# Optimization experiments

Measured on AMD Instinct MI355X. Metric: run time of the kernel, lower is better.

Reference implementation:

```python
import jax, jax.numpy as jnp
import numpy as np

N_NODES = 50000
N_EDGES = 1_250_000
D_FEAT = 64


def setup_inputs() -> dict:
    key = jax.random.key(0)
    k_seq, k_rows, k_cols, k_vals = jax.random.split(key, 4)
    seq = jax.random.normal(k_seq, (1, N_NODES, D_FEAT), dtype=jnp.float32)
    rows = jnp.sort(jax.random.randint(k_rows, (N_EDGES,), 0, N_NODES, dtype=jnp.int32))
    cols = jax.random.randint(k_cols, (N_EDGES,), 0, N_NODES, dtype=jnp.int32)
    vals = jax.random.uniform(k_vals, (N_EDGES,), dtype=jnp.float32)
    return {"seq": seq, "vals": vals, "rows": rows, "cols": cols}


def reference(seq, vals, rows, cols):
    # torch.spmm(adj, seq.squeeze(0)) with adj in COO form (rows, cols, vals):
    # out[r] = sum_{e: rows[e]==r} vals[e] * seq[0, cols[e], :]
    x = jnp.squeeze(seq, 0)                      # [N, D]
    gathered = x[cols] * vals[:, None]           # [E, D] gather + scale
    out = jax.ops.segment_sum(gathered, rows, num_segments=N_NODES)  # [N, D]
    return out[None]                             # unsqueeze(0) -> [1, N, D]
```

## Files before the change

kernel.cpp:

```cpp
#include <hip/hip_runtime.h>


#define WPB 4
#define RPW 8

typedef float  f32x4 __attribute__((ext_vector_type(4)));

__global__ __launch_bounds__(256) void prep_kernel(
    const float4* __restrict__ seq,
    uint2*        __restrict__ seqt,
    const int*    __restrict__ rows,
    int*          __restrict__ row_start,
    int n_nodes, int n_edges, int cvt_blocks)
{
    if ((int)blockIdx.x < cvt_blocks) {
        const int t = blockIdx.x * 256 + threadIdx.x;
        if (t >= n_nodes * 16) return;
        const float4 f = seq[t];
        const unsigned ux = __float_as_uint(f.x), uy = __float_as_uint(f.y);
        const unsigned uz = __float_as_uint(f.z), uw = __float_as_uint(f.w);
        const unsigned bx = (ux + 0x7FFFu + ((ux >> 16) & 1u)) >> 16;
        const unsigned by = (uy + 0x7FFFu + ((uy >> 16) & 1u)) >> 16;
        const unsigned bz = (uz + 0x7FFFu + ((uz >> 16) & 1u)) >> 16;
        const unsigned bw = (uw + 0x7FFFu + ((uw >> 16) & 1u)) >> 16;
        uint2 o;
        o.x = bx | (by << 16);
        o.y = bz | (bw << 16);
        const int n = t >> 4;
        const int h = (t >> 3) & 1;
        const int q = t & 7;
        seqt[(size_t)h * (size_t)n_nodes * 8 + n * 8 + q] = o;
    } else {
        const int e = (blockIdx.x - cvt_blocks) * 256 + threadIdx.x;
        if (e >= n_edges) return;
        const int r    = rows[e];
        const int prev = (e == 0) ? -1 : rows[e - 1];
        for (int t = prev + 1; t <= r; ++t) row_start[t] = e;
        if (e == n_edges - 1)
            for (int t = r + 1; t <= n_nodes; ++t) row_start[t] = n_edges;
    }
}

__global__ __launch_bounds__(256) void spmm_kernel(
    const uint2* __restrict__ seqt,
    const float* __restrict__ vals,
    const int*   __restrict__ cols,
    const int*   __restrict__ row_start,
    float*       __restrict__ out,
    int n_nodes, int n_edges)
{
    const int lane = threadIdx.x & 63;
    const int sub  = lane >> 3;
    const int fl   = lane & 7;

    const int h      = blockIdx.x & 1;
    const int rowblk = blockIdx.x >> 1;
    const int wave   = rowblk * WPB + (threadIdx.x >> 6);

    const int r = wave * RPW + sub;
    if (wave * RPW >= n_nodes) return;
    const bool valid = (r < n_nodes);

    int e = 0, e_end = 0;
    if (valid) {
        e     = row_start[r];
        e_end = row_start[r + 1];
    }

    const uint2* __restrict__ base = seqt + (size_t)h * (size_t)n_nodes * 8;

    float4 acc = make_float4(0.f, 0.f, 0.f, 0.f);

    while (__any(e < e_end)) {
        int cidx = e + fl;
        cidx = (cidx < 0) ? 0 : (cidx >= n_edges ? n_edges - 1 : cidx);
        const int   c = __builtin_nontemporal_load(cols + cidx);
        const float v = __builtin_nontemporal_load(vals + cidx);

        uint2 x[8];
#pragma unroll
        for (int u = 0; u < 8; ++u) {
            const int cu = __shfl(c, (sub << 3) | u);
            if (e + u < e_end)
                x[u] = base[(cu << 3) + fl];
        }
#pragma unroll
        for (int u = 0; u < 8; ++u) {
            const float vu = __shfl(v, (sub << 3) | u);
            if (e + u < e_end) {
                const float f0 = __uint_as_float(x[u].x << 16);
                const float f1 = __uint_as_float(x[u].x & 0xFFFF0000u);
                const float f2 = __uint_as_float(x[u].y << 16);
                const float f3 = __uint_as_float(x[u].y & 0xFFFF0000u);
                acc.x = fmaf(vu, f0, acc.x);
                acc.y = fmaf(vu, f1, acc.y);
                acc.z = fmaf(vu, f2, acc.z);
                acc.w = fmaf(vu, f3, acc.w);
            }
        }
        e += 8;
    }

    if (valid) {
        f32x4 o;
        o.x = acc.x; o.y = acc.y; o.z = acc.z; o.w = acc.w;
        __builtin_nontemporal_store(
            o, (f32x4*)out + ((r << 4) + (h << 3) + fl));
    }
}

extern "C" void kernel_launch(void* const* d_in, const int* in_sizes, int n_in,
                              void* d_out, int out_size, void* d_ws, size_t ws_size,
                              hipStream_t stream) {
    const float* seq  = (const float*)d_in[0];
    const float* vals = (const float*)d_in[1];
    const int*   rows = (const int*)d_in[2];
    const int*   cols = (const int*)d_in[3];
    float*       out  = (float*)d_out;

    const int n_edges = in_sizes[1];
    const int n_nodes = out_size / 64;

    int*   row_start = (int*)d_ws;
    size_t off       = (((size_t)(n_nodes + 1) * 4 + 255) / 256) * 256;
    uint2* seqt      = (uint2*)((char*)d_ws + off);

    {
        const int cvt_blocks = (n_nodes * 16 + 255) / 256;
        const int rp_blocks  = (n_edges + 255) / 256;
        prep_kernel<<<cvt_blocks + rp_blocks, 256, 0, stream>>>(
            (const float4*)seq, seqt, rows, row_start,
            n_nodes, n_edges, cvt_blocks);
    }
    {
        const int rows_per_blk = WPB * RPW;
        const int rowblks      = (n_nodes + rows_per_blk - 1) / rows_per_blk;
        spmm_kernel<<<rowblks * 2, 256, 0, stream>>>(
            seqt, vals, cols, row_start, out, n_nodes, n_edges);
    }
}
```

Measured before the change: 111.1 us.

## Process full 64-feature rows per wave with 16B gathers and prefetched indices

Removes the two-way feature split, so each 8-lane group now gathers a full 128-byte bf16 row with uint4 loads and keeps 8 accumulators. This halves the number of blocks and stops cols/vals and row_start from being read twice. It also software-prefetches the next chunk of column indices and values during the current gather, and makes the seq read nontemporal. The costs are more registers per thread and fewer waves in flight to hide gather latency.

Result: faster. 103.0 us (-7.3%).

```diff
diff --git a/kernel.cpp b/kernel.cpp
--- a/kernel.cpp
+++ b/kernel.cpp
@@ -2,21 +2,20 @@
 
 
 #define WPB 4
-#define RPW 8
 
-typedef float  f32x4 __attribute__((ext_vector_type(4)));
+typedef float f32x4 __attribute__((ext_vector_type(4)));
 
 __global__ __launch_bounds__(256) void prep_kernel(
-    const float4* __restrict__ seq,
-    uint2*        __restrict__ seqt,
-    const int*    __restrict__ rows,
-    int*          __restrict__ row_start,
+    const f32x4* __restrict__ seq,
+    uint2*       __restrict__ seqb,
+    const int*   __restrict__ rows,
+    int*         __restrict__ row_start,
     int n_nodes, int n_edges, int cvt_blocks)
 {
     if ((int)blockIdx.x < cvt_blocks) {
         const int t = blockIdx.x * 256 + threadIdx.x;
         if (t >= n_nodes * 16) return;
-        const float4 f = seq[t];
+        const f32x4 f = __builtin_nontemporal_load(seq + t);
         const unsigned ux = __float_as_uint(f.x), uy = __float_as_uint(f.y);
         const unsigned uz = __float_as_uint(f.z), uw = __float_as_uint(f.w);
         const unsigned bx = (ux + 0x7FFFu + ((ux >> 16) & 1u)) >> 16;
@@ -26,10 +25,7 @@
         uint2 o;
         o.x = bx | (by << 16);
         o.y = bz | (bw << 16);
-        const int n = t >> 4;
-        const int h = (t >> 3) & 1;
-        const int q = t & 7;
-        seqt[(size_t)h * (size_t)n_nodes * 8 + n * 8 + q] = o;
+        seqb[t] = o;
     } else {
         const int e = (blockIdx.x - cvt_blocks) * 256 + threadIdx.x;
         if (e >= n_edges) return;
@@ -42,7 +38,7 @@
 }
 
 __global__ __launch_bounds__(256) void spmm_kernel(
-    const uint2* __restrict__ seqt,
+    const uint4* __restrict__ seqb,
     const float* __restrict__ vals,
     const int*   __restrict__ cols,
     const int*   __restrict__ row_start,
@@ -52,13 +48,10 @@
     const int lane = threadIdx.x & 63;
     const int sub  = lane >> 3;
     const int fl   = lane & 7;
+    const int wave = blockIdx.x * WPB + (threadIdx.x >> 6);
 
-    const int h      = blockIdx.x & 1;
-    const int rowblk = blockIdx.x >> 1;
-    const int wave   = rowblk * WPB + (threadIdx.x >> 6);
-
-    const int r = wave * RPW + sub;
-    if (wave * RPW >= n_nodes) return;
+    const int r = wave * 8 + sub;
+    if (wave * 8 >= n_nodes) return;
     const bool valid = (r < n_nodes);
 
     int e = 0, e_end = 0;
@@ -67,45 +60,57 @@
         e_end = row_start[r + 1];
     }
 
-    const uint2* __restrict__ base = seqt + (size_t)h * (size_t)n_nodes * 8;
+    float acc[8] = {0.f, 0.f, 0.f, 0.f, 0.f, 0.f, 0.f, 0.f};
 
-    float4 acc = make_float4(0.f, 0.f, 0.f, 0.f);
+    int   c_cur;
+    float v_cur;
+    {
+        int cidx = e + fl;
+        if (cidx >= n_edges) cidx = n_edges - 1;
+        c_cur = __builtin_nontemporal_load(cols + cidx);
+        v_cur = __builtin_nontemporal_load(vals + cidx);
+    }
 
     while (__any(e < e_end)) {
-        int cidx = e + fl;
-        cidx = (cidx < 0) ? 0 : (cidx >= n_edges ? n_edges - 1 : cidx);
-        const int   c = __builtin_nontemporal_load(cols + cidx);
-        const float v = __builtin_nontemporal_load(vals + cidx);
+        int nidx = e + 8 + fl;
+        if (nidx >= n_edges) nidx = n_edges - 1;
+        const int   c_nxt = __builtin_nontemporal_load(cols + nidx);
+        const float v_nxt = __builtin_nontemporal_load(vals + nidx);
 
-        uint2 x[8];
+        uint4 x[8];
 #pragma unroll
         for (int u = 0; u < 8; ++u) {
-            const int cu = __shfl(c, (sub << 3) | u);
+            const int cu = __shfl(c_cur, (sub << 3) | u);
             if (e + u < e_end)
-                x[u] = base[(cu << 3) + fl];
+                x[u] = seqb[(cu << 3) + fl];
         }
 #pragma unroll
         for (int u = 0; u < 8; ++u) {
-            const float vu = __shfl(v, (sub << 3) | u);
+            const float vu = __shfl(v_cur, (sub << 3) | u);
             if (e + u < e_end) {
-                const float f0 = __uint_as_float(x[u].x << 16);
-                const float f1 = __uint_as_float(x[u].x & 0xFFFF0000u);
-                const float f2 = __uint_as_float(x[u].y << 16);
-                const float f3 = __uint_as_float(x[u].y & 0xFFFF0000u);
-                acc.x = fmaf(vu, f0, acc.x);
-                acc.y = fmaf(vu, f1, acc.y);
-                acc.z = fmaf(vu, f2, acc.z);
-                acc.w = fmaf(vu, f3, acc.w);
+                const unsigned w0 = x[u].x, w1 = x[u].y, w2 = x[u].z, w3 = x[u].w;
+                acc[0] = fmaf(vu, __uint_as_float(w0 << 16),         acc[0]);
+                acc[1] = fmaf(vu, __uint_as_float(w0 & 0xFFFF0000u), acc[1]);
+                acc[2] = fmaf(vu, __uint_as_float(w1 << 16),         acc[2]);
+                acc[3] = fmaf(vu, __uint_as_float(w1 & 0xFFFF0000u), acc[3]);
+                acc[4] = fmaf(vu, __uint_as_float(w2 << 16),         acc[4]);
+                acc[5] = fmaf(vu, __uint_as_float(w2 & 0xFFFF0000u), acc[5]);
+                acc[6] = fmaf(vu, __uint_as_float(w3 << 16),         acc[6]);
+                acc[7] = fmaf(vu, __uint_as_float(w3 & 0xFFFF0000u), acc[7]);
             }
         }
         e += 8;
+        c_cur = c_nxt;
+        v_cur = v_nxt;
     }
 
     if (valid) {
-        f32x4 o;
-        o.x = acc.x; o.y = acc.y; o.z = acc.z; o.w = acc.w;
-        __builtin_nontemporal_store(
-            o, (f32x4*)out + ((r << 4) + (h << 3) + fl));
+        f32x4 o0, o1;
+        o0.x = acc[0]; o0.y = acc[1]; o0.z = acc[2]; o0.w = acc[3];
+        o1.x = acc[4]; o1.y = acc[5]; o1.z = acc[6]; o1.w = acc[7];
+        f32x4* dst = (f32x4*)out + ((r << 4) + (fl << 1));
+        __builtin_nontemporal_store(o0, dst);
+        __builtin_nontemporal_store(o1, dst + 1);
     }
 }
 
@@ -123,19 +128,20 @@
 
     int*   row_start = (int*)d_ws;
     size_t off       = (((size_t)(n_nodes + 1) * 4 + 255) / 256) * 256;
-    uint2* seqt      = (uint2*)((char*)d_ws + off);
+    uint2* seqb      = (uint2*)((char*)d_ws + off);
 
     {
         const int cvt_blocks = (n_nodes * 16 + 255) / 256;
         const int rp_blocks  = (n_edges + 255) / 256;
         prep_kernel<<<cvt_blocks + rp_blocks, 256, 0, stream>>>(
-            (const float4*)seq, seqt, rows, row_start,
+            (const f32x4*)seq, seqb, rows, row_start,
             n_nodes, n_edges, cvt_blocks);
     }
     {
-        const int rows_per_blk = WPB * RPW;
-        const int rowblks      = (n_nodes + rows_per_blk - 1) / rows_per_blk;
-        spmm_kernel<<<rowblks * 2, 256, 0, stream>>>(
-            seqt, vals, cols, row_start, out, n_nodes, n_edges);
+        const int waves  = (n_nodes + 7) / 8;
+        const int blocks = (waves + WPB - 1) / WPB;
+        spmm_kernel<<<blocks, 256, 0, stream>>>(
+            (const uint4*)seqb, vals, cols, row_start, out,
+            n_nodes, n_edges);
     }
 }
```
